# Kernel optimization log

Measured on AMD Instinct MI355X. Metric: run time of the kernel, lower is better.

The kernel has to match this reference:

```python
import jax, jax.numpy as jnp
import numpy as np

E = 32        # num_local_experts
TOP_K = 4     # num_experts_per_tok
H = 1024      # hidden_size
I = 1024      # intermediate_size (expert_dim)
ALPHA = 1.702
LIMIT = 7.0
B, S = 2, 1024


def setup_inputs() -> dict:
    key = jax.random.key(0)
    ks = jax.random.split(key, 8)
    scale = 0.02
    return {
        "hidden_states": jax.random.normal(ks[0], (B, S, H), dtype=jnp.float32),
        "gate_up_proj": jax.random.normal(ks[1], (E, H, 2 * I), dtype=jnp.float32) * scale,
        "gate_up_proj_bias": jax.random.normal(ks[2], (E, 2 * I), dtype=jnp.float32) * scale,
        "down_proj": jax.random.normal(ks[3], (E, I, H), dtype=jnp.float32) * scale,
        "down_proj_bias": jax.random.normal(ks[4], (E, H), dtype=jnp.float32) * scale,
        "router_weight": jax.random.normal(ks[5], (E, H), dtype=jnp.float32) * scale,
        "router_bias": jax.random.normal(ks[6], (E,), dtype=jnp.float32) * scale,
    }


def reference(hidden_states, gate_up_proj, gate_up_proj_bias, down_proj,
              down_proj_bias, router_weight, router_bias):
    b, s, h = hidden_states.shape
    x = hidden_states.reshape(-1, h)                       # [T, H], T = B*S
    t = x.shape[0]

    # ---- router: linear -> topk -> softmax over topk -> scatter to dense scores
    router_logits = x @ router_weight.T + router_bias      # [T, E]
    top_vals, top_idx = jax.lax.top_k(router_logits, TOP_K)
    top_w = jax.nn.softmax(top_vals, axis=-1)
    router_scores = jnp.zeros_like(router_logits).at[
        jnp.arange(t)[:, None], top_idx].set(top_w)        # [T, E]

    # ---- experts (dense all-expert path, interleaved gate/up columns)
    gate_w = gate_up_proj[..., 0::2]                       # [E, H, I]
    up_w = gate_up_proj[..., 1::2]                         # [E, H, I]
    gate_b = gate_up_proj_bias[..., 0::2]                  # [E, I]
    up_b = gate_up_proj_bias[..., 1::2]                    # [E, I]

    gate = jnp.einsum('th,ehi->eti', x, gate_w) + gate_b[:, None, :]
    up = jnp.einsum('th,ehi->eti', x, up_w) + up_b[:, None, :]
    gate = jnp.minimum(gate, LIMIT)
    up = jnp.clip(up, -LIMIT, LIMIT)
    glu = gate * jax.nn.sigmoid(gate * ALPHA)
    next_states = jnp.einsum('eti,eih->eth', (up + 1.0) * glu, down_proj)
    next_states = next_states + down_proj_bias[:, None, :]  # [E, T, H]

    # ---- combine: weight each expert output by its routing score and sum
    routed = jnp.einsum('eth,te->th', next_states, router_scores)
    return routed.reshape(b, s, h), router_scores
```

## Files before the change

### kernel.cpp

```cpp
#include <hip/hip_runtime.h>
#include <cstdint>
#include <cstddef>

#define E_ 32
#define TOPK_ 4
#define H_ 1024
#define I_ 1024
#define T_ 2048
#define ALPHA_ 1.702f
#define LIMIT_ 7.0f
#define BK_ 32
#define BKP_ 40

typedef __attribute__((ext_vector_type(8))) short s8;
typedef __attribute__((ext_vector_type(4))) float f4;

__device__ __forceinline__ unsigned short f2bf(float f) {
  unsigned int u = __float_as_uint(f);
  return (unsigned short)((u + 0x7fffu + ((u >> 16) & 1u)) >> 16);
}

__global__ __launch_bounds__(128)
void router_kernel(const float* __restrict__ x,
                   const float* __restrict__ rw,
                   const float* __restrict__ rb,
                   float* __restrict__ scores,
                   int* __restrict__ counts,
                   int* __restrict__ tok_list,
                   float* __restrict__ w_list) {
  int t = blockIdx.x;
  int tid = threadIdx.x;
  __shared__ float partial[128];
  __shared__ float logits[E_];
  int e = tid & 31, q = tid >> 5;
  const float* xp = x + (size_t)t * H_;
  const float* wp = rw + (size_t)e * H_ + q * 256;
  float s = 0.f;
  #pragma unroll 8
  for (int h = 0; h < 256; ++h) s += xp[q * 256 + h] * wp[h];
  partial[tid] = s;
  __syncthreads();
  if (tid < 32)
    logits[tid] = partial[tid] + partial[tid + 32] + partial[tid + 64] +
                  partial[tid + 96] + rb[tid];
  __syncthreads();
  if (tid == 0) {
    float l[E_];
    #pragma unroll
    for (int i = 0; i < E_; ++i) l[i] = logits[i];
    int idx[TOPK_]; float v[TOPK_];
    for (int k = 0; k < TOPK_; ++k) {
      int bi = 0; float bv = -1e30f;
      for (int i = 0; i < E_; ++i)
        if (l[i] > bv) { bv = l[i]; bi = i; }
      idx[k] = bi; v[k] = bv; l[bi] = -1e30f;
    }
    float m = v[0], den = 0.f, w[TOPK_];
    for (int k = 0; k < TOPK_; ++k) { w[k] = expf(v[k] - m); den += w[k]; }
    float inv = 1.f / den;
    float* srow = scores + (size_t)t * E_;
    #pragma unroll
    for (int i = 0; i < E_; ++i) srow[i] = 0.f;
    for (int k = 0; k < TOPK_; ++k) {
      float wk = w[k] * inv;
      srow[idx[k]] = wk;
      int pos = atomicAdd(&counts[idx[k]], 1);
      tok_list[idx[k] * T_ + pos] = t * TOPK_ + k;
      w_list[idx[k] * T_ + pos] = wk;
    }
  }
}

__global__ __launch_bounds__(256)
void gateup_mfma(const float* __restrict__ x,
                 const float* __restrict__ gw,
                 const float* __restrict__ gb,
                 const int* __restrict__ counts,
                 const int* __restrict__ tok_list,
                 unsigned short* __restrict__ act) {
  int e = blockIdx.z;
  int cnt = counts[e];
  int t0 = blockIdx.y * 64;
  if (t0 >= cnt) return;
  int itile = blockIdx.x;
  int tid = threadIdx.x;
  int lane = tid & 63;
  int wave = tid >> 6;
  int wm = wave >> 1, wn = wave & 1;

  __shared__ __align__(16) unsigned short Xs[64][BKP_];
  __shared__ __align__(16) unsigned short Wg[128][BKP_];
  __shared__ int toks[64];

  if (tid < 64) {
    int slot = t0 + tid;
    toks[tid] = (slot < cnt) ? tok_list[e * T_ + slot] : -1;
  }
  __syncthreads();

  f4 accg[2][2] = {};
  f4 accu[2][2] = {};

  int arow = tid >> 2;
  int akq  = (tid & 3) * 8;
  int aenc = toks[arow];
  const float* axp = (aenc >= 0) ? (x + (size_t)(aenc >> 2) * H_) : x;
  const float* wbase = gw + (size_t)e * H_ * (2 * I_) + itile * 128;

  int fm = lane & 15, ko = (lane >> 4) * 8;

  for (int k0 = 0; k0 < H_; k0 += BK_) {
    s8 av = {};
    if (aenc >= 0) {
      float4 p0 = *(const float4*)(axp + k0 + akq);
      float4 p1 = *(const float4*)(axp + k0 + akq + 4);
      av[0] = (short)f2bf(p0.x); av[1] = (short)f2bf(p0.y);
      av[2] = (short)f2bf(p0.z); av[3] = (short)f2bf(p0.w);
      av[4] = (short)f2bf(p1.x); av[5] = (short)f2bf(p1.y);
      av[6] = (short)f2bf(p1.z); av[7] = (short)f2bf(p1.w);
    }
    *(s8*)&Xs[arow][akq] = av;
    #pragma unroll
    for (int r = 0; r < 2; ++r) {
      int tau = tid + r * 256;
      int n = tau & 127, koct = tau >> 7;
      const float* wp = wbase + (size_t)(k0 + koct * 8) * (2 * I_) + n;
      s8 bv;
      #pragma unroll
      for (int j = 0; j < 8; ++j)
        bv[j] = (short)f2bf(wp[(size_t)j * (2 * I_)]);
      int drow = (n >> 1) + (n & 1) * 64;
      *(s8*)&Wg[drow][koct * 8] = bv;
    }
    __syncthreads();
    s8 a0 = *(s8*)&Xs[wm * 32 + fm][ko];
    s8 a1 = *(s8*)&Xs[wm * 32 + 16 + fm][ko];
    #pragma unroll
    for (int g = 0; g < 2; ++g) {
      s8 bg = *(s8*)&Wg[wn * 32 + g * 16 + fm][ko];
      s8 bu = *(s8*)&Wg[64 + wn * 32 + g * 16 + fm][ko];
      accg[0][g] = __builtin_amdgcn_mfma_f32_16x16x32_bf16(a0, bg, accg[0][g], 0, 0, 0);
      accg[1][g] = __builtin_amdgcn_mfma_f32_16x16x32_bf16(a1, bg, accg[1][g], 0, 0, 0);
      accu[0][g] = __builtin_amdgcn_mfma_f32_16x16x32_bf16(a0, bu, accu[0][g], 0, 0, 0);
      accu[1][g] = __builtin_amdgcn_mfma_f32_16x16x32_bf16(a1, bu, accu[1][g], 0, 0, 0);
    }
    __syncthreads();
  }

  int rq = lane >> 4;
  #pragma unroll
  for (int g = 0; g < 2; ++g) {
    int i = itile * 64 + wn * 32 + g * 16 + (lane & 15);
    float bg_ = gb[e * 2 * I_ + 2 * i];
    float bu_ = gb[e * 2 * I_ + 2 * i + 1];
    #pragma unroll
    for (int f = 0; f < 2; ++f) {
      #pragma unroll
      for (int r = 0; r < 4; ++r) {
        int m = wm * 32 + f * 16 + rq * 4 + r;
        int enc = toks[m];
        if (enc < 0) continue;
        float gv = accg[f][g][r] + bg_;
        float uv = accu[f][g][r] + bu_;
        gv = fminf(gv, LIMIT_);
        uv = fminf(fmaxf(uv, -LIMIT_), LIMIT_);
        float glu = gv / (1.f + __expf(-ALPHA_ * gv));
        act[(size_t)enc * I_ + i] = f2bf((uv + 1.f) * glu);
      }
    }
  }
}

__global__ __launch_bounds__(256)
void down_mfma(const unsigned short* __restrict__ act,
               const float* __restrict__ dw,
               const float* __restrict__ db,
               const int* __restrict__ counts,
               const int* __restrict__ tok_list,
               const float* __restrict__ w_list,
               float* __restrict__ dsout) {
  int e = blockIdx.z;
  int cnt = counts[e];
  int t0 = blockIdx.y * 64;
  if (t0 >= cnt) return;
  int htile = blockIdx.x;
  int tid = threadIdx.x;
  int lane = tid & 63;
  int wave = tid >> 6;
  int wm = wave >> 1, wn = wave & 1;

  __shared__ __align__(16) unsigned short Xs[64][BKP_];
  __shared__ __align__(16) unsigned short Wd[128][BKP_];
  __shared__ int toks[64];
  __shared__ float tws[64];

  if (tid < 64) {
    int slot = t0 + tid;
    bool ok = slot < cnt;
    toks[tid] = ok ? tok_list[e * T_ + slot] : -1;
    tws[tid]  = ok ? w_list[e * T_ + slot] : 0.f;
  }
  __syncthreads();

  f4 acc[2][4] = {};

  int arow = tid >> 2;
  int akq  = (tid & 3) * 8;
  int aenc = toks[arow];
  const unsigned short* axp = (aenc >= 0) ? (act + (size_t)aenc * I_) : act;
  const float* wbase = dw + (size_t)e * I_ * H_ + htile * 128;

  int fm = lane & 15, ko = (lane >> 4) * 8;

  for (int k0 = 0; k0 < I_; k0 += BK_) {
    s8 av = {};
    if (aenc >= 0) av = *(const s8*)(axp + k0 + akq);
    *(s8*)&Xs[arow][akq] = av;
    #pragma unroll
    for (int r = 0; r < 2; ++r) {
      int tau = tid + r * 256;
      int n = tau & 127, koct = tau >> 7;
      const float* wp = wbase + (size_t)(k0 + koct * 8) * H_ + n;
      s8 bv;
      #pragma unroll
      for (int j = 0; j < 8; ++j)
        bv[j] = (short)f2bf(wp[(size_t)j * H_]);
      *(s8*)&Wd[n][koct * 8] = bv;
    }
    __syncthreads();
    s8 a0 = *(s8*)&Xs[wm * 32 + fm][ko];
    s8 a1 = *(s8*)&Xs[wm * 32 + 16 + fm][ko];
    #pragma unroll
    for (int g = 0; g < 4; ++g) {
      s8 b = *(s8*)&Wd[wn * 64 + g * 16 + fm][ko];
      acc[0][g] = __builtin_amdgcn_mfma_f32_16x16x32_bf16(a0, b, acc[0][g], 0, 0, 0);
      acc[1][g] = __builtin_amdgcn_mfma_f32_16x16x32_bf16(a1, b, acc[1][g], 0, 0, 0);
    }
    __syncthreads();
  }

  int rq = lane >> 4;
  #pragma unroll
  for (int g = 0; g < 4; ++g) {
    int h = htile * 128 + wn * 64 + g * 16 + (lane & 15);
    float bias = db[e * H_ + h];
    #pragma unroll
    for (int f = 0; f < 2; ++f) {
      #pragma unroll
      for (int r = 0; r < 4; ++r) {
        int m = wm * 32 + f * 16 + rq * 4 + r;
        int enc = toks[m];
        if (enc < 0) continue;
        dsout[(size_t)enc * H_ + h] = (acc[f][g][r] + bias) * tws[m];
      }
    }
  }
}

__global__ __launch_bounds__(256)
void combine_kernel(const float* __restrict__ dsout,
                    float* __restrict__ routed) {
  int idx = blockIdx.x * 256 + threadIdx.x;
  int t = idx >> 8;
  int h = (idx & 255) * 4;
  const float* base = dsout + (size_t)t * 4 * H_ + h;
  float4 a = *(const float4*)(base);
  float4 b = *(const float4*)(base + H_);
  float4 c = *(const float4*)(base + 2 * H_);
  float4 d = *(const float4*)(base + 3 * H_);
  float4 o;
  o.x = a.x + b.x + c.x + d.x;
  o.y = a.y + b.y + c.y + d.y;
  o.z = a.z + b.z + c.z + d.z;
  o.w = a.w + b.w + c.w + d.w;
  *(float4*)(routed + (size_t)t * H_ + h) = o;
}

extern "C" void kernel_launch(void* const* d_in, const int* in_sizes, int n_in,
                              void* d_out, int out_size, void* d_ws, size_t ws_size,
                              hipStream_t stream) {
  (void)in_sizes; (void)n_in; (void)out_size; (void)ws_size;
  const float* x    = (const float*)d_in[0];
  const float* gup  = (const float*)d_in[1];
  const float* gupb = (const float*)d_in[2];
  const float* dwn  = (const float*)d_in[3];
  const float* dwnb = (const float*)d_in[4];
  const float* rw   = (const float*)d_in[5];
  const float* rb   = (const float*)d_in[6];

  float* routed = (float*)d_out;
  float* scores = (float*)d_out + (size_t)T_ * H_;

  char* ws = (char*)d_ws;
  int*   counts   = (int*)ws;
  int*   tok_list = (int*)(ws + 256);
  float* w_list   = (float*)(ws + 256 + (size_t)E_ * T_ * 4);
  unsigned short* act = (unsigned short*)(ws + 256 + 2 * (size_t)E_ * T_ * 4);
  float* dsout = (float*)(ws + 256 + 2 * (size_t)E_ * T_ * 4
                          + (size_t)T_ * TOPK_ * I_ * 2);

  hipMemsetAsync(counts, 0, E_ * sizeof(int), stream);

  router_kernel<<<T_, 128, 0, stream>>>(x, rw, rb, scores, counts, tok_list, w_list);
  gateup_mfma<<<dim3(16, 32, 32), 256, 0, stream>>>(x, gup, gupb, counts, tok_list, act);
  down_mfma<<<dim3(8, 32, 32), 256, 0, stream>>>(act, dwn, dwnb, counts, tok_list, w_list, dsout);
  combine_kernel<<<(T_ * H_ / 4) / 256, 256, 0, stream>>>(dsout, routed);
}
```

Baseline: 682.7 us.

## Double-buffer LDS tiles and prefetch next K-chunk into registers in MoE GEMMs

Both the gate/up and down MFMA kernels now keep two LDS buffers and load the next K-chunk's activations and fp32 weights into registers while the MFMAs for the current chunk run. This drops one barrier per iteration and overlaps global load latency with compute. It costs extra registers for the prefetch arrays and twice the shared memory, which may lower occupancy.

```diff
diff --git a/kernel.cpp b/kernel.cpp
--- a/kernel.cpp
+++ b/kernel.cpp
@@ -88,8 +88,8 @@
   int wave = tid >> 6;
   int wm = wave >> 1, wn = wave & 1;
 
-  __shared__ __align__(16) unsigned short Xs[64][BKP_];
-  __shared__ __align__(16) unsigned short Wg[128][BKP_];
+  __shared__ __align__(16) unsigned short Xs[2][64][BKP_];
+  __shared__ __align__(16) unsigned short Wg[2][128][BKP_];
   __shared__ int toks[64];
 
   if (tid < 64) {
@@ -104,47 +104,79 @@
   int arow = tid >> 2;
   int akq  = (tid & 3) * 8;
   int aenc = toks[arow];
-  const float* axp = (aenc >= 0) ? (x + (size_t)(aenc >> 2) * H_) : x;
+  const float* axp = (aenc >= 0) ? (x + (size_t)(aenc >> 2) * H_ + akq) : nullptr;
   const float* wbase = gw + (size_t)e * H_ * (2 * I_) + itile * 128;
+  int n0 = tid & 127, koct0 = tid >> 7;
+  int drow0 = (n0 >> 1) + (n0 & 1) * 64;
+  const float* wp0 = wbase + (size_t)koct0 * 8 * (2 * I_) + n0;
 
   int fm = lane & 15, ko = (lane >> 4) * 8;
 
-  for (int k0 = 0; k0 < H_; k0 += BK_) {
-    s8 av = {};
+  float pA[8];
+  float pB[2][8];
+
+  {
     if (aenc >= 0) {
-      float4 p0 = *(const float4*)(axp + k0 + akq);
-      float4 p1 = *(const float4*)(axp + k0 + akq + 4);
-      av[0] = (short)f2bf(p0.x); av[1] = (short)f2bf(p0.y);
-      av[2] = (short)f2bf(p0.z); av[3] = (short)f2bf(p0.w);
-      av[4] = (short)f2bf(p1.x); av[5] = (short)f2bf(p1.y);
-      av[6] = (short)f2bf(p1.z); av[7] = (short)f2bf(p1.w);
-    }
-    *(s8*)&Xs[arow][akq] = av;
+      float4 q0 = *(const float4*)(axp);
+      float4 q1 = *(const float4*)(axp + 4);
+      pA[0]=q0.x; pA[1]=q0.y; pA[2]=q0.z; pA[3]=q0.w;
+      pA[4]=q1.x; pA[5]=q1.y; pA[6]=q1.z; pA[7]=q1.w;
+    }
     #pragma unroll
     for (int r = 0; r < 2; ++r) {
-      int tau = tid + r * 256;
-      int n = tau & 127, koct = tau >> 7;
-      const float* wp = wbase + (size_t)(k0 + koct * 8) * (2 * I_) + n;
-      s8 bv;
-      #pragma unroll
-      for (int j = 0; j < 8; ++j)
-        bv[j] = (short)f2bf(wp[(size_t)j * (2 * I_)]);
-      int drow = (n >> 1) + (n & 1) * 64;
-      *(s8*)&Wg[drow][koct * 8] = bv;
+      const float* wp = wp0 + (size_t)r * 16 * (2 * I_);
+      #pragma unroll
+      for (int j = 0; j < 8; ++j) pB[r][j] = wp[(size_t)j * (2 * I_)];
+    }
+  }
+
+  int buf = 0;
+  for (int c = 0; c < H_ / BK_; ++c) {
+    {
+      s8 av = {};
+      if (aenc >= 0) {
+        #pragma unroll
+        for (int j = 0; j < 8; ++j) av[j] = (short)f2bf(pA[j]);
+      }
+      *(s8*)&Xs[buf][arow][akq] = av;
+      #pragma unroll
+      for (int r = 0; r < 2; ++r) {
+        s8 bv;
+        #pragma unroll
+        for (int j = 0; j < 8; ++j) bv[j] = (short)f2bf(pB[r][j]);
+        *(s8*)&Wg[buf][drow0][(koct0 + r * 2) * 8] = bv;
+      }
     }
     __syncthreads();
-    s8 a0 = *(s8*)&Xs[wm * 32 + fm][ko];
-    s8 a1 = *(s8*)&Xs[wm * 32 + 16 + fm][ko];
-    #pragma unroll
-    for (int g = 0; g < 2; ++g) {
-      s8 bg = *(s8*)&Wg[wn * 32 + g * 16 + fm][ko];
-      s8 bu = *(s8*)&Wg[64 + wn * 32 + g * 16 + fm][ko];
-      accg[0][g] = __builtin_amdgcn_mfma_f32_16x16x32_bf16(a0, bg, accg[0][g], 0, 0, 0);
-      accg[1][g] = __builtin_amdgcn_mfma_f32_16x16x32_bf16(a1, bg, accg[1][g], 0, 0, 0);
-      accu[0][g] = __builtin_amdgcn_mfma_f32_16x16x32_bf16(a0, bu, accu[0][g], 0, 0, 0);
-      accu[1][g] = __builtin_amdgcn_mfma_f32_16x16x32_bf16(a1, bu, accu[1][g], 0, 0, 0);
-    }
-    __syncthreads();
+    if (c + 1 < H_ / BK_) {
+      int k0 = (c + 1) * BK_;
+      if (aenc >= 0) {
+        float4 q0 = *(const float4*)(axp + k0);
+        float4 q1 = *(const float4*)(axp + k0 + 4);
+        pA[0]=q0.x; pA[1]=q0.y; pA[2]=q0.z; pA[3]=q0.w;
+        pA[4]=q1.x; pA[5]=q1.y; pA[6]=q1.z; pA[7]=q1.w;
+      }
+      #pragma unroll
+      for (int r = 0; r < 2; ++r) {
+        const float* wp = wp0 + (size_t)(k0 + r * 16) * (2 * I_);
+        #pragma unroll
+        for (int j = 0; j < 8; ++j) pB[r][j] = wp[(size_t)j * (2 * I_)];
+      }
+    }
+    {
+      s8 a0 = *(s8*)&Xs[buf][wm * 32 + fm][ko];
+      s8 a1 = *(s8*)&Xs[buf][wm * 32 + 16 + fm][ko];
+      #pragma unroll
+      for (int g = 0; g < 2; ++g) {
+        s8 bg = *(s8*)&Wg[buf][wn * 32 + g * 16 + fm][ko];
+        s8 bu = *(s8*)&Wg[buf][64 + wn * 32 + g * 16 + fm][ko];
+        accg[0][g] = __builtin_amdgcn_mfma_f32_16x16x32_bf16(a0, bg, accg[0][g], 0, 0, 0);
+        accg[1][g] = __builtin_amdgcn_mfma_f32_16x16x32_bf16(a1, bg, accg[1][g], 0, 0, 0);
+        accu[0][g] = __builtin_amdgcn_mfma_f32_16x16x32_bf16(a0, bu, accu[0][g], 0, 0, 0);
+        accu[1][g] = __builtin_amdgcn_mfma_f32_16x16x32_bf16(a1, bu, accu[1][g], 0, 0, 0);
+      }
+    }
+    buf ^= 1;
   }
 
   int rq = lane >> 4;
@@ -189,8 +221,8 @@
   int wave = tid >> 6;
   int wm = wave >> 1, wn = wave & 1;
 
-  __shared__ __align__(16) unsigned short Xs[64][BKP_];
-  __shared__ __align__(16) unsigned short Wd[128][BKP_];
+  __shared__ __align__(16) unsigned short Xs[2][64][BKP_];
+  __shared__ __align__(16) unsigned short Wd[2][128][BKP_];
   __shared__ int toks[64];
   __shared__ float tws[64];
 
@@ -207,36 +239,58 @@
   int arow = tid >> 2;
   int akq  = (tid & 3) * 8;
   int aenc = toks[arow];
-  const unsigned short* axp = (aenc >= 0) ? (act + (size_t)aenc * I_) : act;
+  const unsigned short* axp = (aenc >= 0) ? (act + (size_t)aenc * I_ + akq) : nullptr;
   const float* wbase = dw + (size_t)e * I_ * H_ + htile * 128;
+  int n0 = tid & 127, koct0 = tid >> 7;
+  const float* wp0 = wbase + (size_t)koct0 * 8 * H_ + n0;
 
   int fm = lane & 15, ko = (lane >> 4) * 8;
 
-  for (int k0 = 0; k0 < I_; k0 += BK_) {
-    s8 av = {};
-    if (aenc >= 0) av = *(const s8*)(axp + k0 + akq);
-    *(s8*)&Xs[arow][akq] = av;
+  s8 pA = {};
+  float pB[2][8];
+
+  {
+    if (aenc >= 0) pA = *(const s8*)(axp);
     #pragma unroll
     for (int r = 0; r < 2; ++r) {
-      int tau = tid + r * 256;
-      int n = tau & 127, koct = tau >> 7;
-      const float* wp = wbase + (size_t)(k0 + koct * 8) * H_ + n;
+      const float* wp = wp0 + (size_t)r * 16 * H_;
+      #pragma unroll
+      for (int j = 0; j < 8; ++j) pB[r][j] = wp[(size_t)j * H_];
+    }
+  }
+
+  int buf = 0;
+  for (int c = 0; c < I_ / BK_; ++c) {
+    *(s8*)&Xs[buf][arow][akq] = pA;
+    #pragma unroll
+    for (int r = 0; r < 2; ++r) {
       s8 bv;
       #pragma unroll
-      for (int j = 0; j < 8; ++j)
-        bv[j] = (short)f2bf(wp[(size_t)j * H_]);
-      *(s8*)&Wd[n][koct * 8] = bv;
+      for (int j = 0; j < 8; ++j) bv[j] = (short)f2bf(pB[r][j]);
+      *(s8*)&Wd[buf][n0][(koct0 + r * 2) * 8] = bv;
     }
     __syncthreads();
-    s8 a0 = *(s8*)&Xs[wm * 32 + fm][ko];
-    s8 a1 = *(s8*)&Xs[wm * 32 + 16 + fm][ko];
-    #pragma unroll
-    for (int g = 0; g < 4; ++g) {
-      s8 b = *(s8*)&Wd[wn * 64 + g * 16 + fm][ko];
-      acc[0][g] = __builtin_amdgcn_mfma_f32_16x16x32_bf16(a0, b, acc[0][g], 0, 0, 0);
-      acc[1][g] = __builtin_amdgcn_mfma_f32_16x16x32_bf16(a1, b, acc[1][g], 0, 0, 0);
-    }
-    __syncthreads();
+    if (c + 1 < I_ / BK_) {
+      int k0 = (c + 1) * BK_;
+      if (aenc >= 0) pA = *(const s8*)(axp + k0);
+      #pragma unroll
+      for (int r = 0; r < 2; ++r) {
+        const float* wp = wp0 + (size_t)(k0 + r * 16) * H_;
+        #pragma unroll
+        for (int j = 0; j < 8; ++j) pB[r][j] = wp[(size_t)j * H_];
+      }
+    }
+    {
+      s8 a0 = *(s8*)&Xs[buf][wm * 32 + fm][ko];
+      s8 a1 = *(s8*)&Xs[buf][wm * 32 + 16 + fm][ko];
+      #pragma unroll
+      for (int g = 0; g < 4; ++g) {
+        s8 b = *(s8*)&Wd[buf][wn * 64 + g * 16 + fm][ko];
+        acc[0][g] = __builtin_amdgcn_mfma_f32_16x16x32_bf16(a0, b, acc[0][g], 0, 0, 0);
+        acc[1][g] = __builtin_amdgcn_mfma_f32_16x16x32_bf16(a1, b, acc[1][g], 0, 0, 0);
+      }
+    }
+    buf ^= 1;
   }
 
   int rq = lane >> 4;
```

Measured after the change: 677.0 us. About the same (-0.8%).
